# Kernel optimization log

Measured on AMD Instinct MI355X. Metric: run time of the kernel, lower is better.

Reference implementation:

```python
import jax, jax.numpy as jnp
import numpy as np

TANH_CLIP = 10.0
TEMP = 1.0


def setup_inputs() -> dict:
    key = jax.random.key(0)
    ks = jax.random.split(key, 8)
    B, N, E, H, SC = 1024, 1000, 128, 8, 256
    dk = E // H
    context = jax.random.normal(ks[0], (B, 1, E), dtype=jnp.float32)
    step_context = jax.random.normal(ks[1], (B, 1, SC), dtype=jnp.float32)
    # scale weights so tanh/softmax stay in a sane numeric range
    W_step = jax.random.normal(ks[2], (E, SC), dtype=jnp.float32) * 0.05
    glimpse_K = jax.random.normal(ks[3], (H, B, 1, N, dk), dtype=jnp.float32)
    glimpse_V = jax.random.normal(ks[4], (H, B, 1, N, dk), dtype=jnp.float32)
    logit_K = jax.random.normal(ks[5], (B, 1, N, E), dtype=jnp.float32)
    W_out = jax.random.normal(ks[6], (E, E), dtype=jnp.float32) * 0.05
    mask = jax.random.randint(ks[7], (B, 1, N), 0, 2).astype(bool)
    mask = mask.at[:, :, 0].set(False)  # guarantee at least one feasible node
    return {"context": context, "step_context": step_context, "W_step": W_step,
            "glimpse_K": glimpse_K, "glimpse_V": glimpse_V, "logit_K": logit_K,
            "W_out": W_out, "mask": mask}


def reference(context, step_context, W_step, glimpse_K, glimpse_V, logit_K, W_out, mask):
    B, S, E = context.shape          # S = num_steps = 1
    H = glimpse_K.shape[0]
    dk = E // H
    neg_inf = jnp.float32(-jnp.inf)
    # query = context_node_projected + project_step_context(step_context)
    query = context + jnp.einsum('bsc,ec->bse', step_context, W_step)  # [B,S,E]
    # split heads: glimpse_Q -> [H,B,S,dk] (the singleton q-dim of the torch code is folded)
    Q = query.reshape(B, S, H, dk).transpose(2, 0, 1, 3)
    # compatibility [H,B,S,N]
    compat = jnp.einsum('hbsk,hbsnk->hbsn', Q, glimpse_K) / jnp.sqrt(jnp.float32(dk))
    compat = jnp.where(mask[None], neg_inf, compat)       # mask_inner
    attn = jax.nn.softmax(compat, axis=-1)
    heads = jnp.einsum('hbsn,hbsnk->hbsk', attn, glimpse_V)  # [H,B,S,dk]
    glimpse = heads.transpose(1, 2, 0, 3).reshape(B, S, E)   # concat heads
    glimpse = jnp.einsum('bse,oe->bso', glimpse, W_out)      # project_out
    # logits against logit_K  [B,S,N]
    logits = jnp.einsum('bse,bsne->bsn', glimpse, logit_K) / jnp.sqrt(jnp.float32(E))
    logits = jnp.tanh(logits) * jnp.float32(TANH_CLIP)       # tanh clipping
    logits = jnp.where(mask, neg_inf, logits)                # mask_logits
    log_p = jax.nn.log_softmax(logits / jnp.float32(TEMP), axis=-1)
    return log_p
```

## Files before the change

### kernel.cpp

```cpp
#include <hip/hip_runtime.h>
#include <hip/hip_bf16.h>
#include <math.h>

#define NB  1024
#define NN  1000
#define NE  128
#define NH  8
#define NDK 16
#define NSC 256

__global__ __launch_bounds__(256, 4)
void evrp_decoder_kernel(const float* __restrict__ ctx,
                         const float* __restrict__ stepc,
                         const float* __restrict__ Wstep,
                         const float* __restrict__ gK,
                         const float* __restrict__ gV,
                         const float* __restrict__ lK,
                         const float* __restrict__ Wout,
                         const unsigned char* __restrict__ mask,
                         __hip_bfloat16* __restrict__ out)
{
    const int b = blockIdx.x;
    const int t = threadIdx.x;

    __shared__ __align__(16) float q[NE];
    __shared__ __align__(16) float sc_l[NH * NN];
    __shared__ __align__(16) float g[NE];
    __shared__ __align__(16) float gout[NE];
    __shared__ __align__(16) float red[256];
    __shared__ __align__(16) float ovl[1024];
    __shared__ float mh[NH];
    __shared__ float rinv[NH];
    __shared__ float Mv, Sv;
    __shared__ int mtype;

    if (t == 0) {
        const unsigned int* mi = reinterpret_cast<const unsigned int*>(mask);
        int ok = 1;
        for (int i = 0; i < 64; ++i) ok = ok && (mi[i] <= 1u);
        mtype = ok;
    }

    red[t] = stepc[b * NSC + t];
    __syncthreads();
    const int m_i32 = mtype;
    if (t < NE) {
        float acc = ctx[b * NE + t];
        const float4* w4 = reinterpret_cast<const float4*>(Wstep + t * NSC);
        #pragma unroll 8
        for (int c4 = 0; c4 < NSC / 4; ++c4) {
            float4 w = w4[c4];
            acc += red[c4 * 4 + 0] * w.x + red[c4 * 4 + 1] * w.y +
                   red[c4 * 4 + 2] * w.z + red[c4 * 4 + 3] * w.w;
        }
        q[t] = acc;
    }
    __syncthreads();

    const int* mask_i = reinterpret_cast<const int*>(mask);
    for (int n = t; n < NN; n += 256) {
        bool mk = m_i32 ? (mask_i[b * NN + n] != 0) : (mask[b * NN + n] != 0);
        if (mk) {
            #pragma unroll
            for (int h = 0; h < NH; ++h) sc_l[h * NN + n] = -INFINITY;
        } else {
            #pragma unroll
            for (int h = 0; h < NH; ++h) {
                const float4* k4 = reinterpret_cast<const float4*>(
                    gK + (((size_t)h * NB + b) * NN + n) * NDK);
                const float4* q4 = reinterpret_cast<const float4*>(q + h * NDK);
                float acc = 0.f;
                #pragma unroll
                for (int i = 0; i < 4; ++i) {
                    float4 kv = k4[i];
                    float4 qv = q4[i];
                    acc += kv.x * qv.x + kv.y * qv.y + kv.z * qv.z + kv.w * qv.w;
                }
                sc_l[h * NN + n] = acc * 0.25f;
            }
        }
    }
    __syncthreads();

    {
        const int h = t >> 5, i = t & 31;
        float m = -INFINITY;
        for (int n = i; n < NN; n += 32) m = fmaxf(m, sc_l[h * NN + n]);
        red[t] = m;
        __syncthreads();
        if (t < NH) {
            float mm = -INFINITY;
            for (int i2 = 0; i2 < 32; ++i2) mm = fmaxf(mm, red[t * 32 + i2]);
            mh[t] = mm;
        }
        __syncthreads();
        const float mhh = mh[h];
        float s = 0.f;
        for (int n = i; n < NN; n += 32) {
            float ev = expf(sc_l[h * NN + n] - mhh);
            sc_l[h * NN + n] = ev;
            s += ev;
        }
        red[t] = s;
        __syncthreads();
        if (t < NH) {
            float ss = 0.f;
            for (int i2 = 0; i2 < 32; ++i2) ss += red[t * 32 + i2];
            rinv[t] = 1.0f / ss;
        }
        __syncthreads();
    }

    {
        float4* hp4 = reinterpret_cast<float4*>(ovl);
        const int h = t >> 5, rem = t & 31, kq = rem >> 3, j = rem & 7;
        const float* vbase = gV + (((size_t)h * NB + b) * NN) * NDK + kq * 4;
        float4 acc = {0.f, 0.f, 0.f, 0.f};
        for (int n = j; n < NN; n += 8) {
            float p = sc_l[h * NN + n];
            if (p != 0.f) {
                float4 v = *reinterpret_cast<const float4*>(vbase + (size_t)n * NDK);
                acc.x += p * v.x; acc.y += p * v.y; acc.z += p * v.z; acc.w += p * v.w;
            }
        }
        hp4[(h * 4 + kq) * 8 + j] = acc;
    }
    __syncthreads();
    if (t < NE) {
        const int h = t >> 4, k = t & 15, kq = k >> 2, kc = k & 3;
        float s = 0.f;
        #pragma unroll
        for (int j = 0; j < 8; ++j) s += ovl[((h * 4 + kq) * 8 + j) * 4 + kc];
        g[t] = s * rinv[h];
    }
    __syncthreads();

    if (t < NE) {
        float acc = 0.f;
        const float4* w4 = reinterpret_cast<const float4*>(Wout + t * NE);
        const float4* g4 = reinterpret_cast<const float4*>(g);
        #pragma unroll 8
        for (int e4 = 0; e4 < NE / 4; ++e4) {
            float4 w = w4[e4];
            float4 gg = g4[e4];
            acc += w.x * gg.x + w.y * gg.y + w.z * gg.z + w.w * gg.w;
        }
        gout[t] = acc;
    }
    __syncthreads();

    float* llds = ovl;
    for (int n = t; n < NN; n += 256) {
        bool mk = m_i32 ? (mask_i[b * NN + n] != 0) : (mask[b * NN + n] != 0);
        float val;
        if (mk) {
            val = -INFINITY;
        } else {
            const float4* lk4 = reinterpret_cast<const float4*>(lK + ((size_t)b * NN + n) * NE);
            const float4* go4 = reinterpret_cast<const float4*>(gout);
            float acc = 0.f;
            #pragma unroll 8
            for (int e4 = 0; e4 < NE / 4; ++e4) {
                float4 lv = lk4[e4];
                float4 gv = go4[e4];
                acc += lv.x * gv.x + lv.y * gv.y + lv.z * gv.z + lv.w * gv.w;
            }
            val = tanhf(acc * 0.08838834764831845f) * 10.0f;
        }
        llds[n] = val;
    }
    __syncthreads();

    {
        float m = -INFINITY;
        for (int n = t; n < NN; n += 256) m = fmaxf(m, llds[n]);
        red[t] = m;
        __syncthreads();
        for (int s2 = 128; s2 > 0; s2 >>= 1) {
            if (t < s2) red[t] = fmaxf(red[t], red[t + s2]);
            __syncthreads();
        }
        if (t == 0) Mv = red[0];
        __syncthreads();
        const float M = Mv;
        float s = 0.f;
        for (int n = t; n < NN; n += 256) s += expf(llds[n] - M);
        red[t] = s;
        __syncthreads();
        for (int s2 = 128; s2 > 0; s2 >>= 1) {
            if (t < s2) red[t] += red[t + s2];
            __syncthreads();
        }
        if (t == 0) Sv = logf(red[0]);
        __syncthreads();
        const float LS = M + Sv;
        for (int n = t; n < NN; n += 256) {
            float l = llds[n];
            float r = (l == -INFINITY) ? -3.0e38f : (l - LS);
            out[(size_t)b * NN + n] = __float2bfloat16(r);
        }
    }
}

extern "C" void kernel_launch(void* const* d_in, const int* in_sizes, int n_in,
                              void* d_out, int out_size, void* d_ws, size_t ws_size,
                              hipStream_t stream) {
    const float* ctx   = (const float*)d_in[0];
    const float* stepc = (const float*)d_in[1];
    const float* Wstep = (const float*)d_in[2];
    const float* gK    = (const float*)d_in[3];
    const float* gV    = (const float*)d_in[4];
    const float* lK    = (const float*)d_in[5];
    const float* Wout  = (const float*)d_in[6];
    const unsigned char* mask = (const unsigned char*)d_in[7];
    __hip_bfloat16* out = (__hip_bfloat16*)d_out;

    evrp_decoder_kernel<<<dim3(NB), dim3(256), 0, stream>>>(
        ctx, stepc, Wstep, gK, gV, lK, Wout, mask, out);
}
```

Measured before the change: 256.2 us.

## Split decoder into query, per-head attention, and logits kernels

Breaks the single fused per-batch kernel into three kernels: a query projection, an attention kernel with one block per (head, batch) pair that does the softmax in registers with wavefront shuffles, and a logits/log-softmax kernel. Intermediates pass through the workspace. The goal is more parallelism and smaller LDS use per block, in place of the fused kernel's 32 KB score buffer and strided per-head loops. This costs two extra launches and workspace round-trips, and falls back to the fused kernel when the workspace is too small.

New measurement: 222.7 us. -13.1%, faster.

```diff
diff --git a/kernel.cpp b/kernel.cpp
--- a/kernel.cpp
+++ b/kernel.cpp
@@ -9,20 +9,220 @@
 #define NDK 16
 #define NSC 256
 
+__global__ __launch_bounds__(128)
+void query_kernel(const float* __restrict__ ctx, const float* __restrict__ stepc,
+                  const float* __restrict__ Wstep, float* __restrict__ q_ws)
+{
+    const int b = blockIdx.x, t = threadIdx.x;
+    __shared__ float sc[NSC];
+    sc[t] = stepc[b * NSC + t];
+    sc[t + 128] = stepc[b * NSC + t + 128];
+    __syncthreads();
+    float acc = ctx[b * NE + t];
+    const float4* w4 = reinterpret_cast<const float4*>(Wstep + t * NSC);
+    #pragma unroll 8
+    for (int c4 = 0; c4 < NSC / 4; ++c4) {
+        float4 w = w4[c4];
+        acc += sc[4*c4] * w.x + sc[4*c4+1] * w.y + sc[4*c4+2] * w.z + sc[4*c4+3] * w.w;
+    }
+    q_ws[b * NE + t] = acc;
+}
+
+__global__ __launch_bounds__(256)
+void attn_kernel(const float* __restrict__ q_ws, const float* __restrict__ gK,
+                 const float* __restrict__ gV, const unsigned char* __restrict__ mask,
+                 float* __restrict__ heads_ws)
+{
+    const int bid = blockIdx.x;
+    const int h = bid >> 10;
+    const int b = bid & (NB - 1);
+    const int t = threadIdx.x;
+    const int w = t >> 6, lane = t & 63;
+
+    __shared__ float wmax[4], wsum[4], wred[64];
+    __shared__ int mtype;
+
+    if (t == 0) {
+        const unsigned int* mi = reinterpret_cast<const unsigned int*>(mask);
+        int ok = 1;
+        for (int i = 0; i < 64; ++i) ok = ok && (mi[i] <= 1u);
+        mtype = ok;
+    }
+    __syncthreads();
+    const int m_i32 = mtype;
+    const int* mask_i = reinterpret_cast<const int*>(mask);
+
+    const float4* q4 = reinterpret_cast<const float4*>(q_ws + b * NE + h * NDK);
+    float4 q0 = q4[0], q1 = q4[1], q2 = q4[2], q3 = q4[3];
+
+    const float* Kbase = gK + ((size_t)h * NB + b) * NN * NDK;
+    const float* Vbase = gV + ((size_t)h * NB + b) * NN * NDK;
+
+    float sc[4];
+    #pragma unroll
+    for (int i = 0; i < 4; ++i) {
+        const int n = t + i * 256;
+        float v = -INFINITY;
+        if (n < NN) {
+            bool mk = m_i32 ? (mask_i[b * NN + n] != 0) : (mask[b * NN + n] != 0);
+            if (!mk) {
+                const float4* k4 = reinterpret_cast<const float4*>(Kbase + (size_t)n * NDK);
+                float4 k0 = k4[0], k1 = k4[1], k2 = k4[2], k3 = k4[3];
+                float acc = k0.x*q0.x + k0.y*q0.y + k0.z*q0.z + k0.w*q0.w
+                          + k1.x*q1.x + k1.y*q1.y + k1.z*q1.z + k1.w*q1.w
+                          + k2.x*q2.x + k2.y*q2.y + k2.z*q2.z + k2.w*q2.w
+                          + k3.x*q3.x + k3.y*q3.y + k3.z*q3.z + k3.w*q3.w;
+                v = acc * 0.25f;
+            }
+        }
+        sc[i] = v;
+    }
+
+    float m = fmaxf(fmaxf(sc[0], sc[1]), fmaxf(sc[2], sc[3]));
+    #pragma unroll
+    for (int off = 32; off > 0; off >>= 1) m = fmaxf(m, __shfl_down(m, off));
+    if (lane == 0) wmax[w] = m;
+    __syncthreads();
+    const float M = fmaxf(fmaxf(wmax[0], wmax[1]), fmaxf(wmax[2], wmax[3]));
+
+    float e[4], s = 0.f;
+    #pragma unroll
+    for (int i = 0; i < 4; ++i) { e[i] = expf(sc[i] - M); s += e[i]; }
+    #pragma unroll
+    for (int off = 32; off > 0; off >>= 1) s += __shfl_down(s, off);
+    if (lane == 0) wsum[w] = s;
+    __syncthreads();
+    const float rinv = 1.0f / (wsum[0] + wsum[1] + wsum[2] + wsum[3]);
+
+    float acc[16];
+    #pragma unroll
+    for (int k = 0; k < 16; ++k) acc[k] = 0.f;
+    #pragma unroll
+    for (int i = 0; i < 4; ++i) {
+        const int n = t + i * 256;
+        const float p = e[i];
+        if (n < NN && p != 0.f) {
+            const float4* v4 = reinterpret_cast<const float4*>(Vbase + (size_t)n * NDK);
+            float4 v0 = v4[0], v1 = v4[1], v2 = v4[2], v3 = v4[3];
+            acc[0]+=p*v0.x; acc[1]+=p*v0.y; acc[2]+=p*v0.z; acc[3]+=p*v0.w;
+            acc[4]+=p*v1.x; acc[5]+=p*v1.y; acc[6]+=p*v1.z; acc[7]+=p*v1.w;
+            acc[8]+=p*v2.x; acc[9]+=p*v2.y; acc[10]+=p*v2.z; acc[11]+=p*v2.w;
+            acc[12]+=p*v3.x; acc[13]+=p*v3.y; acc[14]+=p*v3.z; acc[15]+=p*v3.w;
+        }
+    }
+    #pragma unroll
+    for (int k = 0; k < 16; ++k) {
+        float a = acc[k];
+        #pragma unroll
+        for (int off = 32; off > 0; off >>= 1) a += __shfl_down(a, off);
+        acc[k] = a;
+    }
+    if (lane < 16) wred[w * 16 + lane] = acc[lane];
+    __syncthreads();
+    if (lane == 0) {
+        #pragma unroll
+        for (int k = 0; k < 16; ++k) wred[w * 16 + k] = acc[k];
+    }
+    __syncthreads();
+    if (t < NDK) {
+        float r = wred[t] + wred[16 + t] + wred[32 + t] + wred[48 + t];
+        heads_ws[b * NE + h * NDK + t] = r * rinv;
+    }
+}
+
+__global__ __launch_bounds__(256)
+void logits_kernel(const float* __restrict__ heads_ws, const float* __restrict__ Wout,
+                   const float* __restrict__ lK, const unsigned char* __restrict__ mask,
+                   __hip_bfloat16* __restrict__ out)
+{
+    const int b = blockIdx.x, t = threadIdx.x;
+    __shared__ __align__(16) float g[NE];
+    __shared__ __align__(16) float gout[NE];
+    __shared__ __align__(16) float llds[NN];
+    __shared__ __align__(16) float red[256];
+    __shared__ float Mv, Sv;
+    __shared__ int mtype;
+
+    if (t == 0) {
+        const unsigned int* mi = reinterpret_cast<const unsigned int*>(mask);
+        int ok = 1;
+        for (int i = 0; i < 64; ++i) ok = ok && (mi[i] <= 1u);
+        mtype = ok;
+    }
+    if (t < NE) g[t] = heads_ws[b * NE + t];
+    __syncthreads();
+    const int m_i32 = mtype;
+    const int* mask_i = reinterpret_cast<const int*>(mask);
+
+    if (t < NE) {
+        float acc = 0.f;
+        const float4* w4 = reinterpret_cast<const float4*>(Wout + t * NE);
+        const float4* g4 = reinterpret_cast<const float4*>(g);
+        #pragma unroll 8
+        for (int e4 = 0; e4 < NE / 4; ++e4) {
+            float4 wv = w4[e4]; float4 gg = g4[e4];
+            acc += wv.x*gg.x + wv.y*gg.y + wv.z*gg.z + wv.w*gg.w;
+        }
+        gout[t] = acc;
+    }
+    __syncthreads();
+
+    for (int n = t; n < NN; n += 256) {
+        bool mk = m_i32 ? (mask_i[b * NN + n] != 0) : (mask[b * NN + n] != 0);
+        float val;
+        if (mk) {
+            val = -3.0e38f;
+        } else {
+            const float4* lk4 = reinterpret_cast<const float4*>(lK + ((size_t)b * NN + n) * NE);
+            const float4* go4 = reinterpret_cast<const float4*>(gout);
+            float acc = 0.f;
+            #pragma unroll 8
+            for (int e4 = 0; e4 < NE / 4; ++e4) {
+                float4 lv = lk4[e4]; float4 gv = go4[e4];
+                acc += lv.x*gv.x + lv.y*gv.y + lv.z*gv.z + lv.w*gv.w;
+            }
+            val = tanhf(acc * 0.08838834764831845f) * 10.0f;
+        }
+        llds[n] = val;
+    }
+    __syncthreads();
+
+    float m = -INFINITY;
+    for (int n = t; n < NN; n += 256) m = fmaxf(m, llds[n]);
+    red[t] = m;
+    __syncthreads();
+    for (int s2 = 128; s2 > 0; s2 >>= 1) {
+        if (t < s2) red[t] = fmaxf(red[t], red[t + s2]);
+        __syncthreads();
+    }
+    if (t == 0) Mv = red[0];
+    __syncthreads();
+    const float M = Mv;
+    float s = 0.f;
+    for (int n = t; n < NN; n += 256) s += expf(llds[n] - M);
+    red[t] = s;
+    __syncthreads();
+    for (int s2 = 128; s2 > 0; s2 >>= 1) {
+        if (t < s2) red[t] += red[t + s2];
+        __syncthreads();
+    }
+    if (t == 0) Sv = logf(red[0]);
+    __syncthreads();
+    const float LS = M + Sv;
+    for (int n = t; n < NN; n += 256) {
+        out[(size_t)b * NN + n] = __float2bfloat16(llds[n] - LS);
+    }
+}
+
 __global__ __launch_bounds__(256, 4)
-void evrp_decoder_kernel(const float* __restrict__ ctx,
-                         const float* __restrict__ stepc,
-                         const float* __restrict__ Wstep,
-                         const float* __restrict__ gK,
-                         const float* __restrict__ gV,
-                         const float* __restrict__ lK,
-                         const float* __restrict__ Wout,
-                         const unsigned char* __restrict__ mask,
-                         __hip_bfloat16* __restrict__ out)
+void evrp_decoder_fused(const float* __restrict__ ctx, const float* __restrict__ stepc,
+                        const float* __restrict__ Wstep, const float* __restrict__ gK,
+                        const float* __restrict__ gV, const float* __restrict__ lK,
+                        const float* __restrict__ Wout, const unsigned char* __restrict__ mask,
+                        __hip_bfloat16* __restrict__ out)
 {
     const int b = blockIdx.x;
     const int t = threadIdx.x;
-
     __shared__ __align__(16) float q[NE];
     __shared__ __align__(16) float sc_l[NH * NN];
     __shared__ __align__(16) float g[NE];
@@ -40,7 +240,6 @@
         for (int i = 0; i < 64; ++i) ok = ok && (mi[i] <= 1u);
         mtype = ok;
     }
-
     red[t] = stepc[b * NSC + t];
     __syncthreads();
     const int m_i32 = mtype;
@@ -50,13 +249,11 @@
         #pragma unroll 8
         for (int c4 = 0; c4 < NSC / 4; ++c4) {
             float4 w = w4[c4];
-            acc += red[c4 * 4 + 0] * w.x + red[c4 * 4 + 1] * w.y +
-                   red[c4 * 4 + 2] * w.z + red[c4 * 4 + 3] * w.w;
+            acc += red[c4*4+0]*w.x + red[c4*4+1]*w.y + red[c4*4+2]*w.z + red[c4*4+3]*w.w;
         }
         q[t] = acc;
     }
     __syncthreads();
-
     const int* mask_i = reinterpret_cast<const int*>(mask);
     for (int n = t; n < NN; n += 256) {
         bool mk = m_i32 ? (mask_i[b * NN + n] != 0) : (mask[b * NN + n] != 0);
@@ -66,22 +263,19 @@
         } else {
             #pragma unroll
             for (int h = 0; h < NH; ++h) {
-                const float4* k4 = reinterpret_cast<const float4*>(
-                    gK + (((size_t)h * NB + b) * NN + n) * NDK);
+                const float4* k4 = reinterpret_cast<const float4*>(gK + (((size_t)h*NB + b)*NN + n)*NDK);
                 const float4* q4 = reinterpret_cast<const float4*>(q + h * NDK);
                 float acc = 0.f;
                 #pragma unroll
                 for (int i = 0; i < 4; ++i) {
-                    float4 kv = k4[i];
-                    float4 qv = q4[i];
-                    acc += kv.x * qv.x + kv.y * qv.y + kv.z * qv.z + kv.w * qv.w;
+                    float4 kv = k4[i]; float4 qv = q4[i];
+                    acc += kv.x*qv.x + kv.y*qv.y + kv.z*qv.z + kv.w*qv.w;
                 }
                 sc_l[h * NN + n] = acc * 0.25f;
             }
         }
     }
     __syncthreads();
-
     {
         const int h = t >> 5, i = t & 31;
         float m = -INFINITY;
@@ -110,7 +304,6 @@
         }
         __syncthreads();
     }
-
     {
         float4* hp4 = reinterpret_cast<float4*>(ovl);
         const int h = t >> 5, rem = t & 31, kq = rem >> 3, j = rem & 7;
@@ -120,7 +313,7 @@
             float p = sc_l[h * NN + n];
             if (p != 0.f) {
                 float4 v = *reinterpret_cast<const float4*>(vbase + (size_t)n * NDK);
-                acc.x += p * v.x; acc.y += p * v.y; acc.z += p * v.z; acc.w += p * v.w;
+                acc.x += p*v.x; acc.y += p*v.y; acc.z += p*v.z; acc.w += p*v.w;
             }
         }
         hp4[(h * 4 + kq) * 8 + j] = acc;
@@ -134,43 +327,37 @@
         g[t] = s * rinv[h];
     }
     __syncthreads();
-
     if (t < NE) {
         float acc = 0.f;
         const float4* w4 = reinterpret_cast<const float4*>(Wout + t * NE);
         const float4* g4 = reinterpret_cast<const float4*>(g);
         #pragma unroll 8
         for (int e4 = 0; e4 < NE / 4; ++e4) {
-            float4 w = w4[e4];
-            float4 gg = g4[e4];
-            acc += w.x * gg.x + w.y * gg.y + w.z * gg.z + w.w * gg.w;
+            float4 w = w4[e4]; float4 gg = g4[e4];
+            acc += w.x*gg.x + w.y*gg.y + w.z*gg.z + w.w*gg.w;
         }
         gout[t] = acc;
     }
     __syncthreads();
-
     float* llds = ovl;
     for (int n = t; n < NN; n += 256) {
         bool mk = m_i32 ? (mask_i[b * NN + n] != 0) : (mask[b * NN + n] != 0);
         float val;
-        if (mk) {
-            val = -INFINITY;
-        } else {
+        if (mk) val = -INFINITY;
+        else {
             const float4* lk4 = reinterpret_cast<const float4*>(lK + ((size_t)b * NN + n) * NE);
             const float4* go4 = reinterpret_cast<const float4*>(gout);
             float acc = 0.f;
             #pragma unroll 8
             for (int e4 = 0; e4 < NE / 4; ++e4) {
-                float4 lv = lk4[e4];
-                float4 gv = go4[e4];
-                acc += lv.x * gv.x + lv.y * gv.y + lv.z * gv.z + lv.w * gv.w;
+                float4 lv = lk4[e4]; float4 gv = go4[e4];
+                acc += lv.x*gv.x + lv.y*gv.y + lv.z*gv.z + lv.w*gv.w;
             }
             val = tanhf(acc * 0.08838834764831845f) * 10.0f;
         }
         llds[n] = val;
     }
     __syncthreads();
-
     {
         float m = -INFINITY;
         for (int n = t; n < NN; n += 256) m = fmaxf(m, llds[n]);
@@ -215,6 +402,15 @@
     const unsigned char* mask = (const unsigned char*)d_in[7];
     __hip_bfloat16* out = (__hip_bfloat16*)d_out;
 
-    evrp_decoder_kernel<<<dim3(NB), dim3(256), 0, stream>>>(
-        ctx, stepc, Wstep, gK, gV, lK, Wout, mask, out);
+    const size_t need = (size_t)NB * NE * 4 * 2;
+    if (ws_size >= need) {
+        float* q_ws     = (float*)d_ws;
+        float* heads_ws = q_ws + (size_t)NB * NE;
+        query_kernel <<<dim3(NB),      dim3(128), 0, stream>>>(ctx, stepc, Wstep, q_ws);
+        attn_kernel  <<<dim3(NB * NH), dim3(256), 0, stream>>>(q_ws, gK, gV, mask, heads_ws);
+        logits_kernel<<<dim3(NB),      dim3(256), 0, stream>>>(heads_ws, Wout, lK, mask, out);
+    } else {
+        evrp_decoder_fused<<<dim3(NB), dim3(256), 0, stream>>>(
+            ctx, stepc, Wstep, gK, gV, lK, Wout, mask, out);
+    }
 }
```
